# Optimization experiments

Hardware: AMD Instinct MI355X
Metric: run time of the kernel (lower is better)

## Reference

```python
import jax, jax.numpy as jnp
import numpy as np

B, N, C, H, MC, LIE, KD = 2, 2048, 256, 8, 256, 3, 16
DH = C // H

def swish(x):
    return x * jax.nn.sigmoid(x)

def layernorm(x, g, b):
    m = jnp.mean(x, axis=-1, keepdims=True)
    v = jnp.var(x, axis=-1, keepdims=True)
    return (x - m) * jax.lax.rsqrt(v + 1e-5) * g + b

def setup_inputs():
    ks = jax.random.split(jax.random.key(0), 12)
    p = lambda i, shape, s: jax.random.normal(ks[i], shape, jnp.float32) * s
    return dict(
        pairwise_g=jax.random.normal(ks[0], (B, N, N, LIE), jnp.float32),
        x=jax.random.normal(ks[1], (B, N, C), jnp.float32),
        mask=jnp.ones((B, N), dtype=bool),
        ln1_g=jnp.ones((C,), jnp.float32), ln1_b=jnp.zeros((C,), jnp.float32),
        ln2_g=jnp.ones((C,), jnp.float32), ln2_b=jnp.zeros((C,), jnp.float32),
        wn_w1=p(2, (LIE, KD), 0.3), wn_b1=jnp.zeros((KD,), jnp.float32),
        wn_w2=p(3, (KD, KD), 0.3), wn_b2=jnp.zeros((KD,), jnp.float32),
        wn_w3=p(4, (KD, H), 0.3), wn_b3=jnp.zeros((H,), jnp.float32),
        wq=p(5, (C, C), 0.05), bq=jnp.zeros((C,), jnp.float32),
        wk=p(6, (C, C), 0.05), bk=jnp.zeros((C,), jnp.float32),
        in_w=p(7, (C, C), 0.05), in_b=jnp.zeros((C,), jnp.float32),
        out_w=p(8, (C, C), 0.05), out_b=jnp.zeros((C,), jnp.float32),
        mlp_w1=p(9, (C, C), 0.05), mlp_b1=jnp.zeros((C,), jnp.float32),
        mlp_w2=p(10, (C, C), 0.05), mlp_b2=jnp.zeros((C,), jnp.float32),
    )

def _ema(pairwise_g, x, mask, wn_w1, wn_b1, wn_w2, wn_b2, wn_w3, wn_b3,
         wq, bq, wk, bk, in_w, in_b, out_w, out_b):
    b, n, c = x.shape
    # neighbourhood extraction: topk smallest T(3) group distances (mc_samples=MC, fill=1.0)
    dists = jnp.linalg.norm(pairwise_g, axis=-1)                      # (b,n,n)
    dists = jnp.where(mask[:, None, :], dists, jnp.float32(1e8))
    _, idx = jax.lax.top_k(-dists, MC)                                # (b,n,k)
    nbhd_g = jnp.take_along_axis(pairwise_g, idx[..., None], axis=2)  # (b,n,k,LIE)
    nbhd_mask = jnp.take_along_axis(jnp.broadcast_to(mask[:, None, :], (b, n, n)), idx, axis=2)
    # location kernel: MultiheadWeightNet MLP on pairwise group elements -> per-head scalar
    hloc = swish(nbhd_g @ wn_w1 + wn_b1)
    hloc = swish(hloc @ wn_w2 + wn_b2)
    loc = hloc @ wn_w3 + wn_b3                                        # (b,n,k,H)
    # feature kernel: multihead dot product over gathered neighbour keys
    q = (x @ wq + bq).reshape(b, n, H, DH)
    kf = (x @ wk + bk).reshape(b, n, H, DH)
    k_nbhd = jax.vmap(lambda kfb, ib: kfb[ib])(kf, idx)               # (b,n,k,H,DH)
    scores = jnp.einsum('bnhd,bnkhd->bnkh', q, k_nbhd) / jnp.sqrt(jnp.float32(DH))
    pre = jnp.where(nbhd_mask[..., None], loc + scores, jnp.float32(-1e38))
    attn = jax.nn.softmax(pre, axis=2)                                # (b,n,k,H)
    # values; scatter attention into dense (b,n,n,H) exactly as the torch code, then aggregate
    v = (x @ in_w + in_b).reshape(b, n, H, DH)
    BS = jnp.arange(b)[:, None, None]
    NNS = jnp.arange(n)[None, :, None]
    aw = jnp.zeros((b, n, n, H), attn.dtype).at[BS, NNS, idx].set(attn)
    out = jnp.einsum('bnmh,bmhd->bnhd', aw, v).reshape(b, n, c)
    return out @ out_w + out_b

def reference(pairwise_g, x, mask, ln1_g, ln1_b, ln2_g, ln2_b,
              wn_w1, wn_b1, wn_w2, wn_b2, wn_w3, wn_b3,
              wq, bq, wk, bk, in_w, in_b, out_w, out_b,
              mlp_w1, mlp_b1, mlp_w2, mlp_b2):
    # EquivariantTransformerBlock with block_norm='layer_pre'
    x = x + _ema(pairwise_g, layernorm(x, ln1_g, ln1_b), mask,
                 wn_w1, wn_b1, wn_w2, wn_b2, wn_w3, wn_b3,
                 wq, bq, wk, bk, in_w, in_b, out_w, out_b)
    h = layernorm(x, ln2_g, ln2_b)
    x = x + (swish(h @ mlp_w1 + mlp_b1) @ mlp_w2 + mlp_b2)
    return x
```

## Files before the change

kernel.cpp:

```cpp
#include <hip/hip_runtime.h>
#include <hip/hip_bf16.h>

#define Bb 2
#define Nn 2048
#define Cc 256
#define Hh 8
#define MCk 256
#define RT (Bb * Nn)

typedef __hip_bfloat16 bf16;
typedef _Float16 f16;
typedef __fp16 h2v __attribute__((ext_vector_type(2)));
typedef __fp16 h8 __attribute__((ext_vector_type(8)));
typedef float f32x4 __attribute__((ext_vector_type(4)));

__device__ __forceinline__ h2v bc16(unsigned u) { return __builtin_bit_cast(h2v, u); }
__device__ __forceinline__ unsigned bcu(h2v v) { return __builtin_bit_cast(unsigned, v); }

__device__ __forceinline__ float dot2(h2v a, h2v b, float c) {
  return __builtin_amdgcn_fdot2(a, b, c, false);
}
__device__ __forceinline__ f32x4 mfma16(h8 a, h8 b, f32x4 c) {
  return __builtin_amdgcn_mfma_f32_16x16x32_f16(a, b, c, 0, 0, 0);
}
__device__ __forceinline__ float swish_f(float z) {
  return z * __builtin_amdgcn_rcpf(1.f + __expf(-z));
}

__global__ __launch_bounds__(256) void k1_prep_ln_select(
    const float* __restrict__ w0, const float* __restrict__ w1,
    const float* __restrict__ w2, const float* __restrict__ w3,
    const float* __restrict__ w4, const float* __restrict__ w5,
    f16* __restrict__ wtout,
    const float* __restrict__ x, const float* __restrict__ g,
    const float* __restrict__ b, f16* __restrict__ lnout,
    const float* __restrict__ pg, int* __restrict__ idxout)
{
  __shared__ float tile[32][33];
  __shared__ int rc[31][4];
  __shared__ int eqlist[2048];
  __shared__ int nsel, neq;
  int bx = blockIdx.x;
  int t = threadIdx.x;
  if (bx < 384) {
    int wb = bx / 64, tid = bx % 64;
    const float* ws_[6] = {w0, w1, w2, w3, w4, w5};
    const float* W = ws_[wb];
    f16* o = wtout + (size_t)wb * 65536;
    int tn0 = (tid & 7) * 32, tk0 = (tid >> 3) * 32;
    int tl = t & 31, tg = t >> 5;
#pragma unroll
    for (int r = 0; r < 4; r++) {
      int k = tk0 + tg * 4 + r;
      tile[tg * 4 + r][tl] = W[(size_t)k * 256 + tn0 + tl];
    }
    __syncthreads();
#pragma unroll
    for (int r = 0; r < 4; r++) {
      int n = tn0 + tg * 4 + r;
      o[(size_t)n * 256 + tk0 + tl] = (f16)tile[tl][tg * 4 + r];
    }
  } else if (bx < 1408) {
    int wave = t >> 6, lane = t & 63;
    int row = (bx - 384) * 4 + wave;
    const float4 v = reinterpret_cast<const float4*>(x + (size_t)row * Cc)[lane];
    float s  = v.x + v.y + v.z + v.w;
    float s2 = v.x * v.x + v.y * v.y + v.z * v.z + v.w * v.w;
#pragma unroll
    for (int m = 1; m < 64; m <<= 1) {
      s  += __shfl_xor(s, m);
      s2 += __shfl_xor(s2, m);
    }
    float mean = s * (1.0f / Cc);
    float var  = s2 * (1.0f / Cc) - mean * mean;
    float rs   = rsqrtf(var + 1e-5f);
    const float4 gg = reinterpret_cast<const float4*>(g)[lane];
    const float4 bb = reinterpret_cast<const float4*>(b)[lane];
    float ox = (v.x - mean) * rs * gg.x + bb.x;
    float oy = (v.y - mean) * rs * gg.y + bb.y;
    float oz = (v.z - mean) * rs * gg.z + bb.z;
    float ow = (v.w - mean) * rs * gg.w + bb.w;
    uint2 st;
    st.x = bcu(__builtin_amdgcn_cvt_pkrtz(ox, oy));
    st.y = bcu(__builtin_amdgcn_cvt_pkrtz(oz, ow));
    *(uint2*)(lnout + (size_t)row * Cc + lane * 4) = st;
  } else {
    int row = bx - 1408;
    int wave = t >> 6, lane = t & 63;
    const float4* b4 = (const float4*)(pg + (size_t)row * (Nn * 3));
    float4 v0 = b4[6 * t + 0], v1 = b4[6 * t + 1], v2 = b4[6 * t + 2];
    float4 v3 = b4[6 * t + 3], v4 = b4[6 * t + 4], v5 = b4[6 * t + 5];
    unsigned u[8];
    u[0] = __float_as_uint(sqrtf(v0.x * v0.x + v0.y * v0.y + v0.z * v0.z));
    u[1] = __float_as_uint(sqrtf(v0.w * v0.w + v1.x * v1.x + v1.y * v1.y));
    u[2] = __float_as_uint(sqrtf(v1.z * v1.z + v1.w * v1.w + v2.x * v2.x));
    u[3] = __float_as_uint(sqrtf(v2.y * v2.y + v2.z * v2.z + v2.w * v2.w));
    u[4] = __float_as_uint(sqrtf(v3.x * v3.x + v3.y * v3.y + v3.z * v3.z));
    u[5] = __float_as_uint(sqrtf(v3.w * v3.w + v4.x * v4.x + v4.y * v4.y));
    u[6] = __float_as_uint(sqrtf(v4.z * v4.z + v4.w * v4.w + v5.x * v5.x));
    u[7] = __float_as_uint(sqrtf(v5.y * v5.y + v5.z * v5.z + v5.w * v5.w));
    if (t == 0) { nsel = 0; neq = 0; }
    unsigned T = 0;
    for (int bit = 30; bit >= 0; bit--) {
      unsigned cand = T | (1u << bit);
      int c = 0;
#pragma unroll
      for (int jj = 0; jj < 8; jj++) c += __popcll(__ballot(u[jj] < cand));
      if (lane == 0) rc[bit][wave] = c;
      __syncthreads();
      c = rc[bit][0] + rc[bit][1] + rc[bit][2] + rc[bit][3];
      if (c <= MCk - 1) T = cand;
    }
    unsigned long long lmask = (1ull << lane) - 1ull;
#pragma unroll
    for (int jj = 0; jj < 8; jj++) {
      int col = t * 8 + jj;
      bool less = u[jj] < T;
      bool eq   = (u[jj] == T);
      unsigned long long bls = __ballot(less);
      unsigned long long beq = __ballot(eq);
      int cls = __popcll(bls), ceq = __popcll(beq);
      int bl_ = 0, be_ = 0;
      if (lane == 0) {
        bl_ = atomicAdd(&nsel, cls);
        be_ = atomicAdd(&neq, ceq);
      }
      bl_ = __shfl(bl_, 0);
      be_ = __shfl(be_, 0);
      if (less) idxout[(size_t)row * MCk + bl_ + __popcll(bls & lmask)] = col;
      if (eq)   eqlist[be_ + __popcll(beq & lmask)] = col;
    }
    __syncthreads();
    int cl = nsel, nq = neq;
    int need = MCk - cl;
    for (int e = t; e < nq; e += 256) {
      int colE = eqlist[e];
      int rank = 0;
      for (int j = 0; j < nq; j++) rank += (eqlist[j] < colE) ? 1 : 0;
      if (rank < need) idxout[(size_t)row * MCk + cl + rank] = colE;
    }
  }
}

__global__ __launch_bounds__(256) void k2_locmlp_qkv(
    const float* __restrict__ pg, const int* __restrict__ idxb,
    uint4* __restrict__ locout,
    const float* __restrict__ w1, const float* __restrict__ b1,
    const float* __restrict__ w2, const float* __restrict__ b2,
    const float* __restrict__ w3, const float* __restrict__ b3,
    const f16* __restrict__ A,
    const f16* __restrict__ WTq, const float* __restrict__ Bq,
    const f16* __restrict__ WTk, const float* __restrict__ Bk,
    const f16* __restrict__ WTv, const float* __restrict__ Bv,
    f16* __restrict__ outq, f16* __restrict__ outk, f16* __restrict__ outv)
{
  __shared__ float wnl[64];
  __shared__ h2v   w2p[128];
  __shared__ float bn2[16];
  __shared__ h2v   w3p[64];
  __shared__ float bn3[8];
  int t = threadIdx.x;
  if (blockIdx.x < 4096) {
    int row = blockIdx.x;
    for (int i = t; i < 280; i += 256) {
      if (i < 48) {
        wnl[i] = w1[i];
      } else if (i < 64) {
        wnl[i] = b1[i - 48];
      } else if (i < 192) {
        int j = i - 64, i2 = j >> 4, o = j & 15;
        w2p[j] = __builtin_amdgcn_cvt_pkrtz(w2[(2 * i2) * 16 + o], w2[(2 * i2 + 1) * 16 + o]);
      } else if (i < 208) {
        bn2[i - 192] = b2[i - 192];
      } else if (i < 272) {
        int j = i - 208, i2 = j >> 3, o = j & 7;
        w3p[j] = __builtin_amdgcn_cvt_pkrtz(w3[(2 * i2) * 8 + o], w3[(2 * i2 + 1) * 8 + o]);
      } else {
        bn3[i - 272] = b3[i - 272];
      }
    }
    int m = idxb[(size_t)row * 256 + t];
    const float* gsp = pg + ((size_t)row * Nn + m) * 3;
    float g0 = gsp[0], g1 = gsp[1], g2 = gsp[2];
    __syncthreads();
    float h1[16];
#pragma unroll
    for (int o = 0; o < 16; o++) {
      float z = wnl[48 + o] + g0 * wnl[o] + g1 * wnl[16 + o] + g2 * wnl[32 + o];
      h1[o] = swish_f(z);
    }
    h2v hp1[8];
#pragma unroll
    for (int i = 0; i < 8; i++) hp1[i] = __builtin_amdgcn_cvt_pkrtz(h1[2 * i], h1[2 * i + 1]);
    float hh[16];
#pragma unroll
    for (int o = 0; o < 16; o++) {
      float z = bn2[o];
#pragma unroll
      for (int i2 = 0; i2 < 8; i2++) z = dot2(hp1[i2], w2p[i2 * 16 + o], z);
      hh[o] = swish_f(z);
    }
    h2v hp2[8];
#pragma unroll
    for (int i = 0; i < 8; i++) hp2[i] = __builtin_amdgcn_cvt_pkrtz(hh[2 * i], hh[2 * i + 1]);
    float loc[8];
#pragma unroll
    for (int o = 0; o < 8; o++) {
      float z = bn3[o];
#pragma unroll
      for (int i2 = 0; i2 < 8; i2++) z = dot2(hp2[i2], w3p[i2 * 8 + o], z);
      loc[o] = z;
    }
    uint4 lv;
    lv.x = bcu(__builtin_amdgcn_cvt_pkrtz(loc[0], loc[1]));
    lv.y = bcu(__builtin_amdgcn_cvt_pkrtz(loc[2], loc[3]));
    lv.z = bcu(__builtin_amdgcn_cvt_pkrtz(loc[4], loc[5]));
    lv.w = bcu(__builtin_amdgcn_cvt_pkrtz(loc[6], loc[7]));
    locout[(size_t)row * 256 + t] = lv;
  } else {
    int bxq = blockIdx.x - 4096;
    int wid = t >> 6, lane = t & 63;
    int m0 = ((bxq & 63) * 4 + wid) * 16;
    int n0 = (bxq >> 6) * 32;
    int lm = lane & 15, lk = lane >> 4;
    const h8* Ab = (const h8*)(A + (size_t)(m0 + lm) * 256) + lk;
    const h8* Q0 = (const h8*)(WTq + (size_t)(n0 + lm) * 256) + lk;
    const h8* Q1 = (const h8*)(WTq + (size_t)(n0 + 16 + lm) * 256) + lk;
    const h8* K0 = (const h8*)(WTk + (size_t)(n0 + lm) * 256) + lk;
    const h8* K1 = (const h8*)(WTk + (size_t)(n0 + 16 + lm) * 256) + lk;
    const h8* V0 = (const h8*)(WTv + (size_t)(n0 + lm) * 256) + lk;
    const h8* V1 = (const h8*)(WTv + (size_t)(n0 + 16 + lm) * 256) + lk;
    f32x4 aq0 = {0.f,0.f,0.f,0.f}, aq1 = {0.f,0.f,0.f,0.f};
    f32x4 ak0 = {0.f,0.f,0.f,0.f}, ak1 = {0.f,0.f,0.f,0.f};
    f32x4 av0 = {0.f,0.f,0.f,0.f}, av1 = {0.f,0.f,0.f,0.f};
#pragma unroll
    for (int ks = 0; ks < 8; ks++) {
      h8 a = Ab[ks * 4];
      aq0 = mfma16(a, Q0[ks * 4], aq0);
      aq1 = mfma16(a, Q1[ks * 4], aq1);
      ak0 = mfma16(a, K0[ks * 4], ak0);
      ak1 = mfma16(a, K1[ks * 4], ak1);
      av0 = mfma16(a, V0[ks * 4], av0);
      av1 = mfma16(a, V1[ks * 4], av1);
    }
    const float qs = 0.17677669529663687f;
    float bq0 = Bq[n0 + lm], bq1 = Bq[n0 + 16 + lm];
    float bk0 = Bk[n0 + lm], bk1 = Bk[n0 + 16 + lm];
    float bv0 = Bv[n0 + lm], bv1 = Bv[n0 + 16 + lm];
#pragma unroll
    for (int i = 0; i < 4; i++) {
      size_t row = m0 + lk * 4 + i;
      outq[row * 256 + n0 + lm]      = (f16)((aq0[i] + bq0) * qs);
      outq[row * 256 + n0 + 16 + lm] = (f16)((aq1[i] + bq1) * qs);
      outk[row * 256 + n0 + lm]      = (f16)(ak0[i] + bk0);
      outk[row * 256 + n0 + 16 + lm] = (f16)(ak1[i] + bk1);
      outv[row * 256 + n0 + lm]      = (f16)(av0[i] + bv0);
      outv[row * 256 + n0 + 16 + lm] = (f16)(av1[i] + bv1);
    }
  }
}

__global__ __launch_bounds__(256, 4) void attn_kernel(
    const f16* __restrict__ qh, const f16* __restrict__ kh,
    const f16* __restrict__ vv, const int* __restrict__ idxb,
    const uint4* __restrict__ loc16, f16* __restrict__ out)
{
  __shared__ int   offs[256];
  __shared__ float ps[256 * 9];
  __shared__ float agg[4 * 256];
  __shared__ float redmx[4][8];
  __shared__ float redsm[4][8];
  int t = threadIdx.x;
  int row = blockIdx.x;
  int bidx = row >> 11;
  int g = t >> 5, c = t & 31;

  int m = idxb[(size_t)row * 256 + t];
  offs[t] = (bidx * Nn + m) * 512;
  const uint4 qu = *(const uint4*)((const char*)qh + (size_t)row * 512 + (size_t)c * 16);
  h2v q0 = bc16(qu.x), q1 = bc16(qu.y), q2 = bc16(qu.z), q3 = bc16(qu.w);
  const uint4 lv = loc16[(size_t)row * 256 + t];
  __syncthreads();

  int offr[32];
#pragma unroll
  for (int kk = 0; kk < 32; kk++) offr[kk] = offs[kk * 8 + g];

  const char* kbase = (const char*)kh + (size_t)c * 16;
#pragma unroll
  for (int kk = 0; kk < 32; kk += 4) {
    const uint4 k0 = *(const uint4*)(kbase + offr[kk + 0]);
    const uint4 k1 = *(const uint4*)(kbase + offr[kk + 1]);
    const uint4 k2 = *(const uint4*)(kbase + offr[kk + 2]);
    const uint4 k3 = *(const uint4*)(kbase + offr[kk + 3]);
    float p0 = dot2(bc16(k0.x), q0, 0.f);
    float p1 = dot2(bc16(k1.x), q0, 0.f);
    float p2 = dot2(bc16(k2.x), q0, 0.f);
    float p3 = dot2(bc16(k3.x), q0, 0.f);
    p0 = dot2(bc16(k0.y), q1, p0); p1 = dot2(bc16(k1.y), q1, p1);
    p2 = dot2(bc16(k2.y), q1, p2); p3 = dot2(bc16(k3.y), q1, p3);
    p0 = dot2(bc16(k0.z), q2, p0); p1 = dot2(bc16(k1.z), q2, p1);
    p2 = dot2(bc16(k2.z), q2, p2); p3 = dot2(bc16(k3.z), q2, p3);
    p0 = dot2(bc16(k0.w), q3, p0); p1 = dot2(bc16(k1.w), q3, p1);
    p2 = dot2(bc16(k2.w), q3, p2); p3 = dot2(bc16(k3.w), q3, p3);
    p0 += __shfl_xor(p0, 1); p1 += __shfl_xor(p1, 1);
    p2 += __shfl_xor(p2, 1); p3 += __shfl_xor(p3, 1);
    p0 += __shfl_xor(p0, 2); p1 += __shfl_xor(p1, 2);
    p2 += __shfl_xor(p2, 2); p3 += __shfl_xor(p3, 2);
    if ((c & 3) == 0) {
      int hh_ = c >> 2;
      ps[((kk + 0) * 8 + g) * 9 + hh_] = p0;
      ps[((kk + 1) * 8 + g) * 9 + hh_] = p1;
      ps[((kk + 2) * 8 + g) * 9 + hh_] = p2;
      ps[((kk + 3) * 8 + g) * 9 + hh_] = p3;
    }
  }
  __syncthreads();

  h2v l01 = bc16(lv.x), l23 = bc16(lv.y), l45 = bc16(lv.z), l67 = bc16(lv.w);
  float pre[8];
  pre[0] = ps[t * 9 + 0] + (float)l01.x;
  pre[1] = ps[t * 9 + 1] + (float)l01.y;
  pre[2] = ps[t * 9 + 2] + (float)l23.x;
  pre[3] = ps[t * 9 + 3] + (float)l23.y;
  pre[4] = ps[t * 9 + 4] + (float)l45.x;
  pre[5] = ps[t * 9 + 5] + (float)l45.y;
  pre[6] = ps[t * 9 + 6] + (float)l67.x;
  pre[7] = ps[t * 9 + 7] + (float)l67.y;
  float mx[8];
#pragma unroll
  for (int h = 0; h < 8; h++) mx[h] = pre[h];
#pragma unroll
  for (int mm = 1; mm < 64; mm <<= 1) {
#pragma unroll
    for (int h = 0; h < 8; h++) mx[h] = fmaxf(mx[h], __shfl_xor(mx[h], mm));
  }
  int wv = t >> 6, ln = t & 63;
  if (ln == 0) {
#pragma unroll
    for (int h = 0; h < 8; h++) redmx[wv][h] = mx[h];
  }
  __syncthreads();
#pragma unroll
  for (int h = 0; h < 8; h++)
    mx[h] = fmaxf(fmaxf(redmx[0][h], redmx[1][h]), fmaxf(redmx[2][h], redmx[3][h]));
  float e[8], sm[8];
#pragma unroll
  for (int h = 0; h < 8; h++) { e[h] = __expf(pre[h] - mx[h]); sm[h] = e[h]; }
#pragma unroll
  for (int mm = 1; mm < 64; mm <<= 1) {
#pragma unroll
    for (int h = 0; h < 8; h++) sm[h] += __shfl_xor(sm[h], mm);
  }
  if (ln == 0) {
#pragma unroll
    for (int h = 0; h < 8; h++) redsm[wv][h] = sm[h];
  }
  __syncthreads();
#pragma unroll
  for (int h = 0; h < 8; h++) {
    float ssum = redsm[0][h] + redsm[1][h] + redsm[2][h] + redsm[3][h];
    ps[t * 9 + h] = e[h] * __builtin_amdgcn_rcpf(ssum);
  }
  __syncthreads();

  h2v ac0 = {0, 0}, ac1 = {0, 0}, ac2 = {0, 0}, ac3 = {0, 0};
  const char* vbase = (const char*)vv + (size_t)c * 16;
  int hh_ = c >> 2;
#pragma unroll
  for (int kk = 0; kk < 32; kk += 4) {
    const uint4 v0 = *(const uint4*)(vbase + offr[kk + 0]);
    const uint4 v1 = *(const uint4*)(vbase + offr[kk + 1]);
    const uint4 v2 = *(const uint4*)(vbase + offr[kk + 2]);
    const uint4 v3 = *(const uint4*)(vbase + offr[kk + 3]);
    float aw0 = ps[((kk + 0) * 8 + g) * 9 + hh_];
    float aw1 = ps[((kk + 1) * 8 + g) * 9 + hh_];
    float aw2 = ps[((kk + 2) * 8 + g) * 9 + hh_];
    float aw3 = ps[((kk + 3) * 8 + g) * 9 + hh_];
    h2v w0 = __builtin_amdgcn_cvt_pkrtz(aw0, aw0);
    h2v w1 = __builtin_amdgcn_cvt_pkrtz(aw1, aw1);
    h2v w2 = __builtin_amdgcn_cvt_pkrtz(aw2, aw2);
    h2v w3 = __builtin_amdgcn_cvt_pkrtz(aw3, aw3);
    ac0 = bc16(v0.x) * w0 + ac0; ac1 = bc16(v0.y) * w0 + ac1;
    ac2 = bc16(v0.z) * w0 + ac2; ac3 = bc16(v0.w) * w0 + ac3;
    ac0 = bc16(v1.x) * w1 + ac0; ac1 = bc16(v1.y) * w1 + ac1;
    ac2 = bc16(v1.z) * w1 + ac2; ac3 = bc16(v1.w) * w1 + ac3;
    ac0 = bc16(v2.x) * w2 + ac0; ac1 = bc16(v2.y) * w2 + ac1;
    ac2 = bc16(v2.z) * w2 + ac2; ac3 = bc16(v2.w) * w2 + ac3;
    ac0 = bc16(v3.x) * w3 + ac0; ac1 = bc16(v3.y) * w3 + ac1;
    ac2 = bc16(v3.z) * w3 + ac2; ac3 = bc16(v3.w) * w3 + ac3;
  }
  float acc[8] = {(float)ac0.x, (float)ac0.y, (float)ac1.x, (float)ac1.y,
                  (float)ac2.x, (float)ac2.y, (float)ac3.x, (float)ac3.y};
#pragma unroll
  for (int i = 0; i < 8; i++) acc[i] += __shfl_xor(acc[i], 32);
  if ((t & 32) == 0) {
#pragma unroll
    for (int i = 0; i < 8; i++) agg[wv * 256 + c * 8 + i] = acc[i];
  }
  __syncthreads();
  float o = agg[t] + agg[256 + t] + agg[512 + t] + agg[768 + t];
  out[(size_t)row * 256 + t] = (f16)o;
}

__global__ __launch_bounds__(512) void gemm_out_ln(
    const f16* __restrict__ A, const f16* __restrict__ WT,
    const float* __restrict__ bias, const float* __restrict__ xres,
    const float* __restrict__ g, const float* __restrict__ b,
    float* __restrict__ x1, f16* __restrict__ hout)
{
  __shared__ float sred[8][16][2];
  int wid = threadIdx.x >> 6, lane = threadIdx.x & 63;
  int lm = lane & 15, lk = lane >> 4;
  int m0 = blockIdx.x * 16;
  const h8* Ab = (const h8*)(A + (size_t)(m0 + lm) * 256) + lk;
  const h8* Bp0 = (const h8*)(WT + (size_t)(wid * 32 + lm) * 256) + lk;
  const h8* Bp1 = (const h8*)(WT + (size_t)(wid * 32 + 16 + lm) * 256) + lk;
  f32x4 ac0 = {0,0,0,0}, ac1 = {0,0,0,0};
#pragma unroll
  for (int ks = 0; ks < 8; ks++) {
    h8 a = Ab[ks * 4];
    ac0 = mfma16(a, Bp0[ks * 4], ac0);
    ac1 = mfma16(a, Bp1[ks * 4], ac1);
  }
  int c0 = wid * 32 + lm, c1 = wid * 32 + 16 + lm;
  float b0 = bias[c0], b1 = bias[c1];
  float s[4], s2[4];
#pragma unroll
  for (int i = 0; i < 4; i++) {
    size_t row = m0 + lk * 4 + i;
    float y0 = ac0[i] + b0 + xres[row * 256 + c0];
    float y1 = ac1[i] + b1 + xres[row * 256 + c1];
    ac0[i] = y0; ac1[i] = y1;
    x1[row * 256 + c0] = y0;
    x1[row * 256 + c1] = y1;
    s[i] = y0 + y1; s2[i] = y0 * y0 + y1 * y1;
  }
#pragma unroll
  for (int mm = 1; mm < 16; mm <<= 1) {
#pragma unroll
    for (int i = 0; i < 4; i++) {
      s[i]  += __shfl_xor(s[i], mm);
      s2[i] += __shfl_xor(s2[i], mm);
    }
  }
  if (lm == 0) {
#pragma unroll
    for (int i = 0; i < 4; i++) {
      sred[wid][lk * 4 + i][0] = s[i];
      sred[wid][lk * 4 + i][1] = s2[i];
    }
  }
  __syncthreads();
  float g0 = g[c0], g1 = g[c1], bb0 = b[c0], bb1 = b[c1];
#pragma unroll
  for (int i = 0; i < 4; i++) {
    int r = lk * 4 + i;
    float ts = 0.f, ts2 = 0.f;
#pragma unroll
    for (int w = 0; w < 8; w++) { ts += sred[w][r][0]; ts2 += sred[w][r][1]; }
    float mean = ts * (1.f / 256.f);
    float var  = ts2 * (1.f / 256.f) - mean * mean;
    float rs   = rsqrtf(var + 1e-5f);
    size_t row = m0 + r;
    hout[row * 256 + c0] = (f16)((ac0[i] - mean) * rs * g0 + bb0);
    hout[row * 256 + c1] = (f16)((ac1[i] - mean) * rs * g1 + bb1);
  }
}

__global__ __launch_bounds__(512) void mlp_fused(
    const f16* __restrict__ A, const f16* __restrict__ WT1,
    const float* __restrict__ b1, const f16* __restrict__ WT2,
    const float* __restrict__ b2, const float* __restrict__ x1,
    float* __restrict__ outp)
{
  __shared__ f16 hl[16 * 272];
  int wid = threadIdx.x >> 6, lane = threadIdx.x & 63;
  int lm = lane & 15, lk = lane >> 4;
  int m0 = blockIdx.x * 16;
  const h8* Ab = (const h8*)(A + (size_t)(m0 + lm) * 256) + lk;
  const h8* B10 = (const h8*)(WT1 + (size_t)(wid * 32 + lm) * 256) + lk;
  const h8* B11 = (const h8*)(WT1 + (size_t)(wid * 32 + 16 + lm) * 256) + lk;
  const h8* B20 = (const h8*)(WT2 + (size_t)(wid * 32 + lm) * 256) + lk;
  const h8* B21 = (const h8*)(WT2 + (size_t)(wid * 32 + 16 + lm) * 256) + lk;
  f32x4 ac0 = {0,0,0,0}, ac1 = {0,0,0,0};
#pragma unroll
  for (int ks = 0; ks < 8; ks++) {
    h8 a = Ab[ks * 4];
    ac0 = mfma16(a, B10[ks * 4], ac0);
    ac1 = mfma16(a, B11[ks * 4], ac1);
  }
  int c0 = wid * 32 + lm, c1 = wid * 32 + 16 + lm;
  float bb0 = b1[c0], bb1 = b1[c1];
#pragma unroll
  for (int i = 0; i < 4; i++) {
    float y0 = ac0[i] + bb0;
    float y1 = ac1[i] + bb1;
    hl[(lk * 4 + i) * 272 + c0] = (f16)swish_f(y0);
    hl[(lk * 4 + i) * 272 + c1] = (f16)swish_f(y1);
  }
  __syncthreads();
  f32x4 o0 = {0,0,0,0}, o1 = {0,0,0,0};
#pragma unroll
  for (int ks = 0; ks < 8; ks++) {
    h8 a2 = *(const h8*)&hl[lm * 272 + ks * 32 + lk * 8];
    o0 = mfma16(a2, B20[ks * 4], o0);
    o1 = mfma16(a2, B21[ks * 4], o1);
  }
  float d0 = b2[c0], d1 = b2[c1];
#pragma unroll
  for (int i = 0; i < 4; i++) {
    size_t row = m0 + lk * 4 + i;
    outp[row * 256 + c0] = o0[i] + d0 + x1[row * 256 + c0];
    outp[row * 256 + c1] = o1[i] + d1 + x1[row * 256 + c1];
  }
}

extern "C" void kernel_launch(void* const* d_in, const int* in_sizes, int n_in,
                              void* d_out, int out_size, void* d_ws, size_t ws_size,
                              hipStream_t stream)
{
  (void)in_sizes; (void)n_in; (void)out_size; (void)ws_size;
  const float* pg   = (const float*)d_in[0];
  const float* x    = (const float*)d_in[1];
  const float* ln1g = (const float*)d_in[3];
  const float* ln1b = (const float*)d_in[4];
  const float* ln2g = (const float*)d_in[5];
  const float* ln2b = (const float*)d_in[6];
  const float* wnw1 = (const float*)d_in[7];
  const float* wnb1 = (const float*)d_in[8];
  const float* wnw2 = (const float*)d_in[9];
  const float* wnb2 = (const float*)d_in[10];
  const float* wnw3 = (const float*)d_in[11];
  const float* wnb3 = (const float*)d_in[12];
  const float* wq   = (const float*)d_in[13];
  const float* bq   = (const float*)d_in[14];
  const float* wk   = (const float*)d_in[15];
  const float* bk   = (const float*)d_in[16];
  const float* inw  = (const float*)d_in[17];
  const float* inb  = (const float*)d_in[18];
  const float* outw = (const float*)d_in[19];
  const float* outbv= (const float*)d_in[20];
  const float* m1w  = (const float*)d_in[21];
  const float* m1b  = (const float*)d_in[22];
  const float* m2w  = (const float*)d_in[23];
  const float* m2b  = (const float*)d_in[24];

  const size_t RC = (size_t)RT * 256;
  f16*   WTall = (f16*)d_ws;
  f16*   WTq = WTall + 0 * 65536;
  f16*   WTk = WTall + 1 * 65536;
  f16*   WTv = WTall + 2 * 65536;
  f16*   WTo = WTall + 3 * 65536;
  f16*   WTm1= WTall + 4 * 65536;
  f16*   WTm2= WTall + 5 * 65536;
  f16*   ln1h = WTall + 6 * 65536;
  f16*   qh  = ln1h + RC;
  f16*   kh  = qh + RC;
  f16*   vvb = kh + RC;
  int*   idxb= (int*)(vvb + RC);
  f16*   emah= (f16*)(idxb + RC);
  void*  R1  = (void*)(emah + RC);
  uint4* loc16 = (uint4*)R1;
  float* x1    = (float*)R1;
  f16*   ln2h  = ln1h;

  dim3 blk(256);
  k1_prep_ln_select<<<dim3(384 + RT / 4 + RT), blk, 0, stream>>>(
      wq, wk, inw, outw, m1w, m2w, WTall, x, ln1g, ln1b, ln1h, pg, idxb);
  k2_locmlp_qkv<<<dim3(RT + 512), blk, 0, stream>>>(
      pg, idxb, loc16, wnw1, wnb1, wnw2, wnb2, wnw3, wnb3,
      ln1h, WTq, bq, WTk, bk, WTv, inb, qh, kh, vvb);
  attn_kernel<<<dim3(RT), blk, 0, stream>>>(qh, kh, vvb, idxb, loc16, emah);
  gemm_out_ln<<<dim3(RT / 16), dim3(512), 0, stream>>>(emah, WTo, outbv, x, ln2g, ln2b,
                                                       x1, ln2h);
  mlp_fused<<<dim3(RT / 16), dim3(512), 0, stream>>>(ln2h, WTm1, m1b, WTm2, m2b, x1,
                                                     (float*)d_out);
}
```

Baseline: 151.0 us.

## Fuse out-proj/LN2/MLP epilogue and merge softmax reductions in attention

```diff
diff --git a/kernel.cpp b/kernel.cpp
--- a/kernel.cpp
+++ b/kernel.cpp
@@ -288,31 +288,24 @@
 
   const char* kbase = (const char*)kh + (size_t)c * 16;
 #pragma unroll
-  for (int kk = 0; kk < 32; kk += 4) {
-    const uint4 k0 = *(const uint4*)(kbase + offr[kk + 0]);
-    const uint4 k1 = *(const uint4*)(kbase + offr[kk + 1]);
-    const uint4 k2 = *(const uint4*)(kbase + offr[kk + 2]);
-    const uint4 k3 = *(const uint4*)(kbase + offr[kk + 3]);
-    float p0 = dot2(bc16(k0.x), q0, 0.f);
-    float p1 = dot2(bc16(k1.x), q0, 0.f);
-    float p2 = dot2(bc16(k2.x), q0, 0.f);
-    float p3 = dot2(bc16(k3.x), q0, 0.f);
-    p0 = dot2(bc16(k0.y), q1, p0); p1 = dot2(bc16(k1.y), q1, p1);
-    p2 = dot2(bc16(k2.y), q1, p2); p3 = dot2(bc16(k3.y), q1, p3);
-    p0 = dot2(bc16(k0.z), q2, p0); p1 = dot2(bc16(k1.z), q2, p1);
-    p2 = dot2(bc16(k2.z), q2, p2); p3 = dot2(bc16(k3.z), q2, p3);
-    p0 = dot2(bc16(k0.w), q3, p0); p1 = dot2(bc16(k1.w), q3, p1);
-    p2 = dot2(bc16(k2.w), q3, p2); p3 = dot2(bc16(k3.w), q3, p3);
-    p0 += __shfl_xor(p0, 1); p1 += __shfl_xor(p1, 1);
-    p2 += __shfl_xor(p2, 1); p3 += __shfl_xor(p3, 1);
-    p0 += __shfl_xor(p0, 2); p1 += __shfl_xor(p1, 2);
-    p2 += __shfl_xor(p2, 2); p3 += __shfl_xor(p3, 2);
+  for (int kk = 0; kk < 32; kk += 8) {
+    uint4 kr[8];
+#pragma unroll
+    for (int j = 0; j < 8; j++) kr[j] = *(const uint4*)(kbase + offr[kk + j]);
+    float p[8];
+#pragma unroll
+    for (int j = 0; j < 8; j++) {
+      p[j] = dot2(bc16(kr[j].x), q0, 0.f);
+      p[j] = dot2(bc16(kr[j].y), q1, p[j]);
+      p[j] = dot2(bc16(kr[j].z), q2, p[j]);
+      p[j] = dot2(bc16(kr[j].w), q3, p[j]);
+      p[j] += __shfl_xor(p[j], 1);
+      p[j] += __shfl_xor(p[j], 2);
+    }
     if ((c & 3) == 0) {
       int hh_ = c >> 2;
-      ps[((kk + 0) * 8 + g) * 9 + hh_] = p0;
-      ps[((kk + 1) * 8 + g) * 9 + hh_] = p1;
-      ps[((kk + 2) * 8 + g) * 9 + hh_] = p2;
-      ps[((kk + 3) * 8 + g) * 9 + hh_] = p3;
+#pragma unroll
+      for (int j = 0; j < 8; j++) ps[((kk + j) * 8 + g) * 9 + hh_] = p[j];
     }
   }
   __syncthreads();
@@ -335,32 +328,27 @@
 #pragma unroll
     for (int h = 0; h < 8; h++) mx[h] = fmaxf(mx[h], __shfl_xor(mx[h], mm));
   }
+  float e[8], sm[8];
+#pragma unroll
+  for (int h = 0; h < 8; h++) { e[h] = __expf(pre[h] - mx[h]); sm[h] = e[h]; }
+#pragma unroll
+  for (int mm = 1; mm < 64; mm <<= 1) {
+#pragma unroll
+    for (int h = 0; h < 8; h++) sm[h] += __shfl_xor(sm[h], mm);
+  }
   int wv = t >> 6, ln = t & 63;
   if (ln == 0) {
 #pragma unroll
-    for (int h = 0; h < 8; h++) redmx[wv][h] = mx[h];
-  }
-  __syncthreads();
-#pragma unroll
-  for (int h = 0; h < 8; h++)
-    mx[h] = fmaxf(fmaxf(redmx[0][h], redmx[1][h]), fmaxf(redmx[2][h], redmx[3][h]));
-  float e[8], sm[8];
-#pragma unroll
-  for (int h = 0; h < 8; h++) { e[h] = __expf(pre[h] - mx[h]); sm[h] = e[h]; }
-#pragma unroll
-  for (int mm = 1; mm < 64; mm <<= 1) {
-#pragma unroll
-    for (int h = 0; h < 8; h++) sm[h] += __shfl_xor(sm[h], mm);
-  }
-  if (ln == 0) {
-#pragma unroll
-    for (int h = 0; h < 8; h++) redsm[wv][h] = sm[h];
+    for (int h = 0; h < 8; h++) { redmx[wv][h] = mx[h]; redsm[wv][h] = sm[h]; }
   }
   __syncthreads();
 #pragma unroll
   for (int h = 0; h < 8; h++) {
-    float ssum = redsm[0][h] + redsm[1][h] + redsm[2][h] + redsm[3][h];
-    ps[t * 9 + h] = e[h] * __builtin_amdgcn_rcpf(ssum);
+    float m0_ = redmx[0][h], m1_ = redmx[1][h], m2_ = redmx[2][h], m3_ = redmx[3][h];
+    float gm = fmaxf(fmaxf(m0_, m1_), fmaxf(m2_, m3_));
+    float gs = redsm[0][h] * __expf(m0_ - gm) + redsm[1][h] * __expf(m1_ - gm)
+             + redsm[2][h] * __expf(m2_ - gm) + redsm[3][h] * __expf(m3_ - gm);
+    ps[t * 9 + h] = e[h] * __expf(mx[h] - gm) * __builtin_amdgcn_rcpf(gs);
   }
   __syncthreads();
 
@@ -368,27 +356,19 @@
   const char* vbase = (const char*)vv + (size_t)c * 16;
   int hh_ = c >> 2;
 #pragma unroll
-  for (int kk = 0; kk < 32; kk += 4) {
-    const uint4 v0 = *(const uint4*)(vbase + offr[kk + 0]);
-    const uint4 v1 = *(const uint4*)(vbase + offr[kk + 1]);
-    const uint4 v2 = *(const uint4*)(vbase + offr[kk + 2]);
-    const uint4 v3 = *(const uint4*)(vbase + offr[kk + 3]);
-    float aw0 = ps[((kk + 0) * 8 + g) * 9 + hh_];
-    float aw1 = ps[((kk + 1) * 8 + g) * 9 + hh_];
-    float aw2 = ps[((kk + 2) * 8 + g) * 9 + hh_];
-    float aw3 = ps[((kk + 3) * 8 + g) * 9 + hh_];
-    h2v w0 = __builtin_amdgcn_cvt_pkrtz(aw0, aw0);
-    h2v w1 = __builtin_amdgcn_cvt_pkrtz(aw1, aw1);
-    h2v w2 = __builtin_amdgcn_cvt_pkrtz(aw2, aw2);
-    h2v w3 = __builtin_amdgcn_cvt_pkrtz(aw3, aw3);
-    ac0 = bc16(v0.x) * w0 + ac0; ac1 = bc16(v0.y) * w0 + ac1;
-    ac2 = bc16(v0.z) * w0 + ac2; ac3 = bc16(v0.w) * w0 + ac3;
-    ac0 = bc16(v1.x) * w1 + ac0; ac1 = bc16(v1.y) * w1 + ac1;
-    ac2 = bc16(v1.z) * w1 + ac2; ac3 = bc16(v1.w) * w1 + ac3;
-    ac0 = bc16(v2.x) * w2 + ac0; ac1 = bc16(v2.y) * w2 + ac1;
-    ac2 = bc16(v2.z) * w2 + ac2; ac3 = bc16(v2.w) * w2 + ac3;
-    ac0 = bc16(v3.x) * w3 + ac0; ac1 = bc16(v3.y) * w3 + ac1;
-    ac2 = bc16(v3.z) * w3 + ac2; ac3 = bc16(v3.w) * w3 + ac3;
+  for (int kk = 0; kk < 32; kk += 8) {
+    uint4 vr[8];
+#pragma unroll
+    for (int j = 0; j < 8; j++) vr[j] = *(const uint4*)(vbase + offr[kk + j]);
+#pragma unroll
+    for (int j = 0; j < 8; j++) {
+      float aw = ps[((kk + j) * 8 + g) * 9 + hh_];
+      h2v w = __builtin_amdgcn_cvt_pkrtz(aw, aw);
+      ac0 = bc16(vr[j].x) * w + ac0;
+      ac1 = bc16(vr[j].y) * w + ac1;
+      ac2 = bc16(vr[j].z) * w + ac2;
+      ac3 = bc16(vr[j].w) * w + ac3;
+    }
   }
   float acc[8] = {(float)ac0.x, (float)ac0.y, (float)ac1.x, (float)ac1.y,
                   (float)ac2.x, (float)ac2.y, (float)ac3.x, (float)ac3.y};
@@ -403,37 +383,41 @@
   out[(size_t)row * 256 + t] = (f16)o;
 }
 
-__global__ __launch_bounds__(512) void gemm_out_ln(
-    const f16* __restrict__ A, const f16* __restrict__ WT,
-    const float* __restrict__ bias, const float* __restrict__ xres,
+__global__ __launch_bounds__(512) void epilogue(
+    const f16* __restrict__ A, const f16* __restrict__ WTo,
+    const float* __restrict__ bo, const float* __restrict__ xres,
     const float* __restrict__ g, const float* __restrict__ b,
-    float* __restrict__ x1, f16* __restrict__ hout)
+    const f16* __restrict__ WT1, const float* __restrict__ b1,
+    const f16* __restrict__ WT2, const float* __restrict__ b2,
+    float* __restrict__ outp)
 {
   __shared__ float sred[8][16][2];
+  __shared__ f16 hl[16 * 272];
+  __shared__ f16 hl2[16 * 272];
   int wid = threadIdx.x >> 6, lane = threadIdx.x & 63;
   int lm = lane & 15, lk = lane >> 4;
   int m0 = blockIdx.x * 16;
-  const h8* Ab = (const h8*)(A + (size_t)(m0 + lm) * 256) + lk;
-  const h8* Bp0 = (const h8*)(WT + (size_t)(wid * 32 + lm) * 256) + lk;
-  const h8* Bp1 = (const h8*)(WT + (size_t)(wid * 32 + 16 + lm) * 256) + lk;
+  int c0 = wid * 32 + lm, c1 = c0 + 16;
+
+  const h8* Ab  = (const h8*)(A + (size_t)(m0 + lm) * 256) + lk;
+  const h8* Bo0 = (const h8*)(WTo + (size_t)c0 * 256) + lk;
+  const h8* Bo1 = (const h8*)(WTo + (size_t)c1 * 256) + lk;
   f32x4 ac0 = {0,0,0,0}, ac1 = {0,0,0,0};
 #pragma unroll
   for (int ks = 0; ks < 8; ks++) {
     h8 a = Ab[ks * 4];
-    ac0 = mfma16(a, Bp0[ks * 4], ac0);
-    ac1 = mfma16(a, Bp1[ks * 4], ac1);
-  }
-  int c0 = wid * 32 + lm, c1 = wid * 32 + 16 + lm;
-  float b0 = bias[c0], b1 = bias[c1];
+    ac0 = mfma16(a, Bo0[ks * 4], ac0);
+    ac1 = mfma16(a, Bo1[ks * 4], ac1);
+  }
+  float bo0 = bo[c0], bo1 = bo[c1];
+  float xr0[4], xr1[4];
   float s[4], s2[4];
 #pragma unroll
   for (int i = 0; i < 4; i++) {
     size_t row = m0 + lk * 4 + i;
-    float y0 = ac0[i] + b0 + xres[row * 256 + c0];
-    float y1 = ac1[i] + b1 + xres[row * 256 + c1];
-    ac0[i] = y0; ac1[i] = y1;
-    x1[row * 256 + c0] = y0;
-    x1[row * 256 + c1] = y1;
+    float y0 = ac0[i] + bo0 + xres[row * 256 + c0];
+    float y1 = ac1[i] + bo1 + xres[row * 256 + c1];
+    xr0[i] = y0; xr1[i] = y1;
     s[i] = y0 + y1; s2[i] = y0 * y0 + y1 * y1;
   }
 #pragma unroll
@@ -462,57 +446,44 @@
     float mean = ts * (1.f / 256.f);
     float var  = ts2 * (1.f / 256.f) - mean * mean;
     float rs   = rsqrtf(var + 1e-5f);
-    size_t row = m0 + r;
-    hout[row * 256 + c0] = (f16)((ac0[i] - mean) * rs * g0 + bb0);
-    hout[row * 256 + c1] = (f16)((ac1[i] - mean) * rs * g1 + bb1);
-  }
-}
-
-__global__ __launch_bounds__(512) void mlp_fused(
-    const f16* __restrict__ A, const f16* __restrict__ WT1,
-    const float* __restrict__ b1, const f16* __restrict__ WT2,
-    const float* __restrict__ b2, const float* __restrict__ x1,
-    float* __restrict__ outp)
-{
-  __shared__ f16 hl[16 * 272];
-  int wid = threadIdx.x >> 6, lane = threadIdx.x & 63;
-  int lm = lane & 15, lk = lane >> 4;
-  int m0 = blockIdx.x * 16;
-  const h8* Ab = (const h8*)(A + (size_t)(m0 + lm) * 256) + lk;
-  const h8* B10 = (const h8*)(WT1 + (size_t)(wid * 32 + lm) * 256) + lk;
-  const h8* B11 = (const h8*)(WT1 + (size_t)(wid * 32 + 16 + lm) * 256) + lk;
-  const h8* B20 = (const h8*)(WT2 + (size_t)(wid * 32 + lm) * 256) + lk;
-  const h8* B21 = (const h8*)(WT2 + (size_t)(wid * 32 + 16 + lm) * 256) + lk;
-  f32x4 ac0 = {0,0,0,0}, ac1 = {0,0,0,0};
-#pragma unroll
-  for (int ks = 0; ks < 8; ks++) {
-    h8 a = Ab[ks * 4];
-    ac0 = mfma16(a, B10[ks * 4], ac0);
-    ac1 = mfma16(a, B11[ks * 4], ac1);
-  }
-  int c0 = wid * 32 + lm, c1 = wid * 32 + 16 + lm;
-  float bb0 = b1[c0], bb1 = b1[c1];
-#pragma unroll
-  for (int i = 0; i < 4; i++) {
-    float y0 = ac0[i] + bb0;
-    float y1 = ac1[i] + bb1;
-    hl[(lk * 4 + i) * 272 + c0] = (f16)swish_f(y0);
-    hl[(lk * 4 + i) * 272 + c1] = (f16)swish_f(y1);
-  }
-  __syncthreads();
-  f32x4 o0 = {0,0,0,0}, o1 = {0,0,0,0};
+    hl[r * 272 + c0] = (f16)((xr0[i] - mean) * rs * g0 + bb0);
+    hl[r * 272 + c1] = (f16)((xr1[i] - mean) * rs * g1 + bb1);
+  }
+  __syncthreads();
+
+  const h8* B10 = (const h8*)(WT1 + (size_t)c0 * 256) + lk;
+  const h8* B11 = (const h8*)(WT1 + (size_t)c1 * 256) + lk;
+  f32x4 m10 = {0,0,0,0}, m11 = {0,0,0,0};
 #pragma unroll
   for (int ks = 0; ks < 8; ks++) {
     h8 a2 = *(const h8*)&hl[lm * 272 + ks * 32 + lk * 8];
-    o0 = mfma16(a2, B20[ks * 4], o0);
-    o1 = mfma16(a2, B21[ks * 4], o1);
-  }
-  float d0 = b2[c0], d1 = b2[c1];
+    m10 = mfma16(a2, B10[ks * 4], m10);
+    m11 = mfma16(a2, B11[ks * 4], m11);
+  }
+  float b10 = b1[c0], b11 = b1[c1];
+#pragma unroll
+  for (int i = 0; i < 4; i++) {
+    int r = lk * 4 + i;
+    hl2[r * 272 + c0] = (f16)swish_f(m10[i] + b10);
+    hl2[r * 272 + c1] = (f16)swish_f(m11[i] + b11);
+  }
+  __syncthreads();
+
+  const h8* B20 = (const h8*)(WT2 + (size_t)c0 * 256) + lk;
+  const h8* B21 = (const h8*)(WT2 + (size_t)c1 * 256) + lk;
+  f32x4 o0 = {0,0,0,0}, o1 = {0,0,0,0};
+#pragma unroll
+  for (int ks = 0; ks < 8; ks++) {
+    h8 a3 = *(const h8*)&hl2[lm * 272 + ks * 32 + lk * 8];
+    o0 = mfma16(a3, B20[ks * 4], o0);
+    o1 = mfma16(a3, B21[ks * 4], o1);
+  }
+  float b20 = b2[c0], b21 = b2[c1];
 #pragma unroll
   for (int i = 0; i < 4; i++) {
     size_t row = m0 + lk * 4 + i;
-    outp[row * 256 + c0] = o0[i] + d0 + x1[row * 256 + c0];
-    outp[row * 256 + c1] = o1[i] + d1 + x1[row * 256 + c1];
+    outp[row * 256 + c0] = o0[i] + b20 + xr0[i];
+    outp[row * 256 + c1] = o1[i] + b21 + xr1[i];
   }
 }
 
@@ -560,10 +531,7 @@
   f16*   vvb = kh + RC;
   int*   idxb= (int*)(vvb + RC);
   f16*   emah= (f16*)(idxb + RC);
-  void*  R1  = (void*)(emah + RC);
-  uint4* loc16 = (uint4*)R1;
-  float* x1    = (float*)R1;
-  f16*   ln2h  = ln1h;
+  uint4* loc16 = (uint4*)(emah + RC);
 
   dim3 blk(256);
   k1_prep_ln_select<<<dim3(384 + RT / 4 + RT), blk, 0, stream>>>(
@@ -572,8 +540,6 @@
       pg, idxb, loc16, wnw1, wnb1, wnw2, wnb2, wnw3, wnb3,
       ln1h, WTq, bq, WTk, bk, WTv, inb, qh, kh, vvb);
   attn_kernel<<<dim3(RT), blk, 0, stream>>>(qh, kh, vvb, idxb, loc16, emah);
-  gemm_out_ln<<<dim3(RT / 16), dim3(512), 0, stream>>>(emah, WTo, outbv, x, ln2g, ln2b,
-                                                       x1, ln2h);
-  mlp_fused<<<dim3(RT / 16), dim3(512), 0, stream>>>(ln2h, WTm1, m1b, WTm2, m2b, x1,
-                                                     (float*)d_out);
-}
+  epilogue<<<dim3(RT / 16), dim3(512), 0, stream>>>(
+      emah, WTo, outbv, x, ln2g, ln2b, WTm1, m1b, WTm2, m2b, (float*)d_out);
+}
```

Result: slower. 156.5 us (+3.6%).
